# Optimization experiments

Hardware: AMD Instinct MI355X
Metric: run time of the kernel (lower is better)

The kernel has to match this reference:

```python
import jax, jax.numpy as jnp
import numpy as np

ALPHA = 1.0
RANK = 4


def _conv2d_same(x, w):
    # x: [B,C,H,W], w: [O,C,kh,kw], stride 1, 'same' padding
    return jax.lax.conv_general_dilated(
        x, w, window_strides=(1, 1), padding='SAME',
        dimension_numbers=('NCHW', 'OIHW', 'NCHW'))


def setup_inputs() -> dict:
    key = jax.random.key(0)
    k1, k2, k3, k4, k5 = jax.random.split(key, 5)
    B, C, H, W = 32, 64, 64, 256
    O, E, r, k = 64, 4, RANK, 3
    x = jax.random.normal(k1, (B, C, H, W), dtype=jnp.float32)
    subject_id = jax.random.randint(k2, (B,), 0, E, dtype=jnp.int64)
    W_conv = jax.random.normal(k3, (O, C, k, k), dtype=jnp.float32) * (1.0 / np.sqrt(C * k * k))
    W_A = jax.random.normal(k4, (E, r, C, k, k), dtype=jnp.float32) * 0.02
    # torch init zeros W_B; use random here so the LoRA path is numerically exercised
    W_B = jax.random.normal(k5, (E, O, r), dtype=jnp.float32) * 0.02
    return {'x': x, 'subject_id': subject_id, 'W_conv': W_conv, 'W_A': W_A, 'W_B': W_B}


def reference(x, subject_id, W_conv, W_A, W_B):
    B, C, H, W = x.shape
    E, r = W_A.shape[0], W_A.shape[1]
    k = W_A.shape[-1]
    # Base conv
    out = _conv2d_same(x, W_conv)  # [B,O,H,W]
    # Run all adapter A-convs in one batched conv (E*r tiny output channels),
    # then per-sample select the adapter matching subject_id (same math as the
    # masked per-adapter dispatch in the original).
    a_all = _conv2d_same(x, W_A.reshape(E * r, C, k, k))  # [B,E*r,H,W]
    a_all = a_all.reshape(B, E, r, H, W)
    idx = subject_id[:, None, None, None, None]
    a_sel = jnp.take_along_axis(a_all, idx, axis=1)[:, 0]  # [B,r,H,W]
    wb_sel = W_B[subject_id]  # [B,O,r] (1x1 conv weight per sample)
    lora = (ALPHA / r) * jnp.einsum('bor,brhw->bohw', wb_sel, a_sel)
    return out + lora
```

## Files before the change

kernel.cpp:

```cpp
#include <hip/hip_runtime.h>
#include <hip/hip_bf16.h>

typedef __attribute__((ext_vector_type(8)))  short bf16x8;
typedef __attribute__((ext_vector_type(16))) float f32x16;

constexpr int Bn = 32, Cn = 64, Hn = 64, Wn = 256, On = 64, En = 4, Rn = 4;
constexpr float SCALE = 1.0f / Rn;

constexpr int WTILE  = 128;
constexpr int HSTRIP = 8;
constexpr int SLOT_B = 130 * 128;
constexpr int EPI_OS = 12;

__global__ __launch_bounds__(256) void merge_k(
    const float* __restrict__ Wc, const float* __restrict__ Wa,
    const float* __restrict__ Wb, __hip_bfloat16* __restrict__ Wfrag)
{
    int t = blockIdx.x * 256 + threadIdx.x;
    int j    = t & 7;
    int lane = (t >> 3) & 63;
    int g    = t >> 9;
    int s    = g % 36;
    int mh   = (g / 36) & 1;
    int e    = g / 72;
    int m = lane & 31, half = lane >> 5;
    int o = mh * 32 + m;
    int tap = s >> 2, cq = s & 3;
    int c = cq * 16 + half * 8 + j;
    float acc = Wc[(o * Cn + c) * 9 + tap];
#pragma unroll
    for (int r = 0; r < Rn; ++r)
        acc += SCALE * Wb[(e * On + o) * Rn + r] * Wa[((e * Rn + r) * Cn + c) * 9 + tap];
    Wfrag[t] = __float2bfloat16(acc);
}

__global__ __launch_bounds__(256, 2) void conv3_k(
    const float* __restrict__ x, const int* __restrict__ sid,
    const __hip_bfloat16* __restrict__ Wfrag, float* __restrict__ out)
{
    __shared__ __align__(16) char  xs[4 * SLOT_B];
    __shared__ __align__(16) float ep[4 * 64 * EPI_OS];

    const int tid = threadIdx.x;
    const int w0  = blockIdx.x * WTILE;
    const int h0  = blockIdx.y * HSTRIP;
    const int b   = blockIdx.z;
    const int e   = sid[b];

    const int lane = tid & 63, wave = tid >> 6;
    const int mh = wave & 1, nh = wave >> 1;
    const int n = lane & 31, half = lane >> 5;

    bf16x8 wf[36];
    const bf16x8* wg = reinterpret_cast<const bf16x8*>(Wfrag) + (size_t)(e * 2 + mh) * 36 * 64;
#pragma unroll
    for (int s = 0; s < 36; ++s) wf[s] = wg[s * 64 + lane];

    float* epw = ep + wave * 64 * EPI_OS;

    const int cb = tid >> 5;
    const int q  = tid & 31;
    const int side = (tid >> 3) & 1;
    const int hcb  = tid & 7;
    const float* xbase = x + ((size_t)b * Cn + cb * 8) * (size_t)(Hn * Wn) + w0 + 4 * q;
    const int gwh = side ? (w0 + WTILE) : (w0 - 1);
    const bool hv = (unsigned)gwh < (unsigned)Wn;
    const float* hbase = x + ((size_t)b * Cn + hcb * 8) * (size_t)(Hn * Wn) + gwh;

    float4 f[8];
    float  hx[8];

    auto stage_load = [&](int rx) {
        const int gh = h0 + rx;
        if ((unsigned)gh < (unsigned)Hn) {
            const float* src = xbase + (size_t)gh * Wn;
#pragma unroll
            for (int r = 0; r < 8; ++r)
                f[r] = *reinterpret_cast<const float4*>(src + (size_t)r * Hn * Wn);
            if (tid < 16) {
                if (hv) {
                    const float* hs = hbase + (size_t)gh * Wn;
#pragma unroll
                    for (int i = 0; i < 8; ++i) hx[i] = hs[(size_t)i * Hn * Wn];
                } else {
#pragma unroll
                    for (int i = 0; i < 8; ++i) hx[i] = 0.0f;
                }
            }
        } else {
            float4 z4 = make_float4(0.0f, 0.0f, 0.0f, 0.0f);
#pragma unroll
            for (int r = 0; r < 8; ++r) f[r] = z4;
            if (tid < 16) {
#pragma unroll
                for (int i = 0; i < 8; ++i) hx[i] = 0.0f;
            }
        }
    };
    auto stage_store = [&](int rx) {
        const int slot = (rx + 1) & 3;
        char* dbase = xs + slot * SLOT_B;
#pragma unroll
        for (int j = 0; j < 4; ++j) {
            union { __hip_bfloat16 u[8]; bf16x8 v; } pk;
#pragma unroll
            for (int r = 0; r < 8; ++r) {
                float v = (j == 0) ? f[r].x : (j == 1) ? f[r].y : (j == 2) ? f[r].z : f[r].w;
                pk.u[r] = __float2bfloat16(v);
            }
            int ww = 4 * q + 1 + j;
            *reinterpret_cast<bf16x8*>(dbase + ww * 128 + ((cb ^ (ww & 7)) * 16)) = pk.v;
        }
        if (tid < 16) {
            union { __hip_bfloat16 u[8]; bf16x8 v; } pk;
#pragma unroll
            for (int i = 0; i < 8; ++i) pk.u[i] = __float2bfloat16(hx[i]);
            int ww = side ? (WTILE + 1) : 0;
            *reinterpret_cast<bf16x8*>(dbase + ww * 128 + ((hcb ^ (ww & 7)) * 16)) = pk.v;
        }
    };

    stage_load(-1); stage_store(-1);
    stage_load(0);  stage_store(0);
    stage_load(1);  stage_store(1);
    __syncthreads();

    for (int st = 0; st < HSTRIP; ++st) {
        const bool do_stage = (st + 2 <= HSTRIP);
        if (do_stage) stage_load(st + 2);

        f32x16 a[2];
#pragma unroll
        for (int nf = 0; nf < 2; ++nf)
#pragma unroll
            for (int i = 0; i < 16; ++i) a[nf][i] = 0.0f;

#pragma unroll
        for (int s = 0; s < 36; ++s) {
            const int tap = s >> 2, cq = s & 3;
            const int dh = tap / 3, dw = tap % 3;
            const int slotbase = ((st + dh) & 3) * SLOT_B;
#pragma unroll
            for (int nf = 0; nf < 2; ++nf) {
                int ww = nh * 64 + nf * 32 + n + dw;
                int off = slotbase + ww * 128 + (((cq * 2 + half) ^ (ww & 7)) * 16);
                bf16x8 bf = *reinterpret_cast<const bf16x8*>(xs + off);
                a[nf] = __builtin_amdgcn_mfma_f32_32x32x16_bf16(wf[s], bf, a[nf], 0, 0, 0);
            }
        }

        const int hrow = h0 + st;
#pragma unroll
        for (int t4 = 0; t4 < 4; ++t4) {
#pragma unroll
            for (int nf = 0; nf < 2; ++nf) {
                float4 v = make_float4(a[nf][4 * t4 + 0], a[nf][4 * t4 + 1],
                                       a[nf][4 * t4 + 2], a[nf][4 * t4 + 3]);
                *reinterpret_cast<float4*>(&epw[(nf * 32 + n) * EPI_OS + half * 4]) = v;
            }
#pragma unroll
            for (int k = 0; k < 4; ++k) {
                int mrel = 2 * k + half;
                int wbuf = 2 * n;
                float lo = epw[wbuf * EPI_OS + mrel];
                float hi = epw[(wbuf + 1) * EPI_OS + mrel];
                int o = mh * 32 + 8 * t4 + mrel;
                size_t oidx = (((size_t)b * On + o) * Hn + hrow) * Wn + w0 + nh * 64 + wbuf;
                float2 v2; v2.x = lo; v2.y = hi;
                *reinterpret_cast<float2*>(&out[oidx]) = v2;
            }
        }

        if (do_stage) stage_store(st + 2);

        __syncthreads();
    }
}

extern "C" void kernel_launch(void* const* d_in, const int* in_sizes, int n_in,
                              void* d_out, int out_size, void* d_ws, size_t ws_size,
                              hipStream_t stream)
{
    const float* x   = (const float*)d_in[0];
    const int*   sid = (const int*)d_in[1];
    const float* Wc  = (const float*)d_in[2];
    const float* Wa  = (const float*)d_in[3];
    const float* Wb  = (const float*)d_in[4];
    float*       out = (float*)d_out;

    __hip_bfloat16* Wfrag = (__hip_bfloat16*)d_ws;

    merge_k<<<En * 2 * 36 * 64 * 8 / 256, 256, 0, stream>>>(Wc, Wa, Wb, Wfrag);

    dim3 grid(Wn / WTILE, Hn / HSTRIP, Bn);
    conv3_k<<<grid, 256, 0, stream>>>(x, sid, Wfrag, out);
}
```

Measured before the change: 305.9 us.

## Drop LDS epilogue staging, store MFMA accumulators directly, change swizzle and halo split

Removes the shared-memory epilogue buffer and writes MFMA accumulator registers straight to global memory, with each 32-lane row storing contiguous floats per output channel. The LDS swizzle now uses (ww>>2)&7, and the halo columns are loaded by 32 threads with 4 channels each instead of 16 threads with 8. The barrier becomes an explicit lgkmcnt wait plus s_barrier, so it no longer waits on outstanding global memory operations. Direct stores are scalar 4-byte writes rather than float2, which could reduce store efficiency, but they avoid LDS round-trips and the epilogue's LDS traffic.

```diff
diff --git a/kernel.cpp b/kernel.cpp
--- a/kernel.cpp
+++ b/kernel.cpp
@@ -10,7 +10,10 @@
 constexpr int WTILE  = 128;
 constexpr int HSTRIP = 8;
 constexpr int SLOT_B = 130 * 128;
-constexpr int EPI_OS = 12;
+
+__device__ __forceinline__ int swz(int ww, int cb) {
+    return ww * 128 + ((cb ^ ((ww >> 2) & 7)) * 16);
+}
 
 __global__ __launch_bounds__(256) void merge_k(
     const float* __restrict__ Wc, const float* __restrict__ Wa,
@@ -34,18 +37,18 @@
     Wfrag[t] = __float2bfloat16(acc);
 }
 
-__global__ __launch_bounds__(256, 2) void conv3_k(
+__global__ __launch_bounds__(256, 2) void conv4_k(
     const float* __restrict__ x, const int* __restrict__ sid,
     const __hip_bfloat16* __restrict__ Wfrag, float* __restrict__ out)
 {
-    __shared__ __align__(16) char  xs[4 * SLOT_B];
-    __shared__ __align__(16) float ep[4 * 64 * EPI_OS];
+    __shared__ __align__(16) char xs[4 * SLOT_B];
 
     const int tid = threadIdx.x;
     const int w0  = blockIdx.x * WTILE;
     const int h0  = blockIdx.y * HSTRIP;
     const int b   = blockIdx.z;
     const int e   = sid[b];
+    const size_t HW = (size_t)Hn * Wn;
 
     const int lane = tid & 63, wave = tid >> 6;
     const int mh = wave & 1, nh = wave >> 1;
@@ -56,19 +59,19 @@
 #pragma unroll
     for (int s = 0; s < 36; ++s) wf[s] = wg[s * 64 + lane];
 
-    float* epw = ep + wave * 64 * EPI_OS;
-
     const int cb = tid >> 5;
     const int q  = tid & 31;
-    const int side = (tid >> 3) & 1;
-    const int hcb  = tid & 7;
-    const float* xbase = x + ((size_t)b * Cn + cb * 8) * (size_t)(Hn * Wn) + w0 + 4 * q;
-    const int gwh = side ? (w0 + WTILE) : (w0 - 1);
-    const bool hv = (unsigned)gwh < (unsigned)Wn;
-    const float* hbase = x + ((size_t)b * Cn + hcb * 8) * (size_t)(Hn * Wn) + gwh;
+    const float* xbase = x + ((size_t)b * Cn + cb * 8) * HW + w0 + 4 * q;
+
+    const int hside = tid >> 4;
+    const int hidx  = tid & 15;
+    const int hcb   = hidx >> 1, hhi = hidx & 1;
+    const int gwh   = hside ? (w0 + WTILE) : (w0 - 1);
+    const bool hv   = (unsigned)gwh < (unsigned)Wn;
+    const float* hbase = x + ((size_t)b * Cn + hcb * 8 + hhi * 4) * HW + gwh;
 
     float4 f[8];
-    float  hx[8];
+    float  hx[4];
 
     auto stage_load = [&](int rx) {
         const int gh = h0 + rx;
@@ -76,25 +79,23 @@
             const float* src = xbase + (size_t)gh * Wn;
 #pragma unroll
             for (int r = 0; r < 8; ++r)
-                f[r] = *reinterpret_cast<const float4*>(src + (size_t)r * Hn * Wn);
-            if (tid < 16) {
+                f[r] = *reinterpret_cast<const float4*>(src + r * HW);
+            if (tid < 32) {
                 if (hv) {
                     const float* hs = hbase + (size_t)gh * Wn;
 #pragma unroll
-                    for (int i = 0; i < 8; ++i) hx[i] = hs[(size_t)i * Hn * Wn];
+                    for (int i = 0; i < 4; ++i) hx[i] = hs[i * HW];
                 } else {
 #pragma unroll
-                    for (int i = 0; i < 8; ++i) hx[i] = 0.0f;
+                    for (int i = 0; i < 4; ++i) hx[i] = 0.0f;
                 }
             }
         } else {
             float4 z4 = make_float4(0.0f, 0.0f, 0.0f, 0.0f);
 #pragma unroll
             for (int r = 0; r < 8; ++r) f[r] = z4;
-            if (tid < 16) {
 #pragma unroll
-                for (int i = 0; i < 8; ++i) hx[i] = 0.0f;
-            }
+            for (int i = 0; i < 4; ++i) hx[i] = 0.0f;
         }
     };
     auto stage_store = [&](int rx) {
@@ -109,21 +110,26 @@
                 pk.u[r] = __float2bfloat16(v);
             }
             int ww = 4 * q + 1 + j;
-            *reinterpret_cast<bf16x8*>(dbase + ww * 128 + ((cb ^ (ww & 7)) * 16)) = pk.v;
+            *reinterpret_cast<bf16x8*>(dbase + swz(ww, cb)) = pk.v;
         }
-        if (tid < 16) {
-            union { __hip_bfloat16 u[8]; bf16x8 v; } pk;
+        if (tid < 32) {
+            union { __hip_bfloat16 u[4]; short4 v; } pk;
 #pragma unroll
-            for (int i = 0; i < 8; ++i) pk.u[i] = __float2bfloat16(hx[i]);
-            int ww = side ? (WTILE + 1) : 0;
-            *reinterpret_cast<bf16x8*>(dbase + ww * 128 + ((hcb ^ (ww & 7)) * 16)) = pk.v;
+            for (int i = 0; i < 4; ++i) pk.u[i] = __float2bfloat16(hx[i]);
+            int ww = hside ? (WTILE + 1) : 0;
+            *reinterpret_cast<short4*>(dbase + swz(ww, hcb) + hhi * 8) = pk.v;
         }
+    };
+
+    auto barrier = [&]() {
+        asm volatile("s_waitcnt lgkmcnt(0)" ::: "memory");
+        __builtin_amdgcn_s_barrier();
     };
 
     stage_load(-1); stage_store(-1);
     stage_load(0);  stage_store(0);
     stage_load(1);  stage_store(1);
-    __syncthreads();
+    barrier();
 
     for (int st = 0; st < HSTRIP; ++st) {
         const bool do_stage = (st + 2 <= HSTRIP);
@@ -143,37 +149,27 @@
 #pragma unroll
             for (int nf = 0; nf < 2; ++nf) {
                 int ww = nh * 64 + nf * 32 + n + dw;
-                int off = slotbase + ww * 128 + (((cq * 2 + half) ^ (ww & 7)) * 16);
-                bf16x8 bf = *reinterpret_cast<const bf16x8*>(xs + off);
+                bf16x8 bf = *reinterpret_cast<const bf16x8*>(xs + slotbase + swz(ww, cq * 2 + half));
                 a[nf] = __builtin_amdgcn_mfma_f32_32x32x16_bf16(wf[s], bf, a[nf], 0, 0, 0);
             }
         }
 
-        const int hrow = h0 + st;
+        {
+            const int hrow = h0 + st;
+            size_t base = ((size_t)(b * On + mh * 32 + 4 * half) * Hn + hrow) * Wn
+                          + w0 + nh * 64 + n;
 #pragma unroll
-        for (int t4 = 0; t4 < 4; ++t4) {
+            for (int nf = 0; nf < 2; ++nf)
 #pragma unroll
-            for (int nf = 0; nf < 2; ++nf) {
-                float4 v = make_float4(a[nf][4 * t4 + 0], a[nf][4 * t4 + 1],
-                                       a[nf][4 * t4 + 2], a[nf][4 * t4 + 3]);
-                *reinterpret_cast<float4*>(&epw[(nf * 32 + n) * EPI_OS + half * 4]) = v;
-            }
-#pragma unroll
-            for (int k = 0; k < 4; ++k) {
-                int mrel = 2 * k + half;
-                int wbuf = 2 * n;
-                float lo = epw[wbuf * EPI_OS + mrel];
-                float hi = epw[(wbuf + 1) * EPI_OS + mrel];
-                int o = mh * 32 + 8 * t4 + mrel;
-                size_t oidx = (((size_t)b * On + o) * Hn + hrow) * Wn + w0 + nh * 64 + wbuf;
-                float2 v2; v2.x = lo; v2.y = hi;
-                *reinterpret_cast<float2*>(&out[oidx]) = v2;
-            }
+                for (int r = 0; r < 16; ++r) {
+                    int o_off = (r & 3) + 8 * (r >> 2);
+                    out[base + (size_t)o_off * HW + nf * 32] = a[nf][r];
+                }
         }
 
         if (do_stage) stage_store(st + 2);
 
-        __syncthreads();
+        barrier();
     }
 }
 
@@ -193,5 +189,5 @@
     merge_k<<<En * 2 * 36 * 64 * 8 / 256, 256, 0, stream>>>(Wc, Wa, Wb, Wfrag);
 
     dim3 grid(Wn / WTILE, Hn / HSTRIP, Bn);
-    conv3_k<<<grid, 256, 0, stream>>>(x, sid, Wfrag, out);
+    conv4_k<<<grid, 256, 0, stream>>>(x, sid, Wfrag, out);
 }
```

After: 273.3 us. 1.12x faster.
